# Performance work log

Hardware: AMD Instinct MI355X
Metric: run time of the kernel (lower is better)

## Reference

```python
import jax, jax.numpy as jnp
import numpy as np

N_NODES = 50000
N_EDGES = 3200000
N_GRAPHS = 50
IN_FEATS, HIDDEN, OUT_FEATS = 5, 64, 2


def setup_inputs() -> dict:
    key = jax.random.key(0)
    ks = jax.random.split(key, 10)
    x = jax.random.normal(ks[0], (N_NODES, IN_FEATS), dtype=jnp.float32)
    edge_index = jax.random.randint(ks[1], (2, N_EDGES), 0, N_NODES, dtype=jnp.int64)
    edge_attr = jax.random.uniform(ks[2], (N_EDGES, 1), dtype=jnp.float32)
    batch = jnp.sort(jax.random.randint(ks[3], (N_NODES,), 0, N_GRAPHS, dtype=jnp.int64))
    s1 = 1.0 / np.sqrt(IN_FEATS)
    s2 = 1.0 / np.sqrt(HIDDEN)
    W1 = jax.random.uniform(ks[4], (IN_FEATS, HIDDEN), jnp.float32, -s1, s1)
    b1 = jnp.zeros((HIDDEN,), jnp.float32)
    W2 = jax.random.uniform(ks[5], (HIDDEN, HIDDEN), jnp.float32, -s2, s2)
    b2 = jnp.zeros((HIDDEN,), jnp.float32)
    Wo = jax.random.uniform(ks[6], (HIDDEN, OUT_FEATS), jnp.float32, -s2, s2)
    bo = jax.random.uniform(ks[7], (OUT_FEATS,), jnp.float32, -s2, s2)
    return {"x": x, "edge_index": edge_index, "edge_attr": edge_attr, "batch": batch,
            "W1": W1, "b1": b1, "W2": W2, "b2": b2, "Wo": Wo, "bo": bo}


def _gcn_conv(x, src, dst, ew, W, b):
    # symmetric normalization: D^{-1/2} (A + I) D^{-1/2}, weighted degrees
    deg = jax.ops.segment_sum(ew, dst, num_segments=N_NODES)
    dinv = jnp.where(deg > 0, jax.lax.rsqrt(jnp.where(deg > 0, deg, 1.0)), 0.0)
    norm = dinv[src] * ew * dinv[dst]  # [E+N]
    h = x @ W                           # transform before propagate (PyG order)
    msg = h[src] * norm[:, None]        # gather + scale per edge
    out = jax.ops.segment_sum(msg, dst, num_segments=N_NODES)
    return out + b


def reference(x, edge_index, edge_attr, batch, W1, b1, W2, b2, Wo, bo):
    ew = edge_attr.squeeze(-1)
    loop = jnp.arange(N_NODES, dtype=edge_index.dtype)  # add self-loops (GCNConv default)
    src = jnp.concatenate([edge_index[0], loop])
    dst = jnp.concatenate([edge_index[1], loop])
    ew = jnp.concatenate([ew, jnp.ones((N_NODES,), ew.dtype)])
    h = jax.nn.relu(_gcn_conv(x, src, dst, ew, W1, b1))
    h = jax.nn.relu(_gcn_conv(h, src, dst, ew, W2, b2))
    # global mean pool over graphs
    sums = jax.ops.segment_sum(h, batch, num_segments=N_GRAPHS)
    cnt = jax.ops.segment_sum(jnp.ones((N_NODES,), h.dtype), batch, num_segments=N_GRAPHS)
    pooled = sums / jnp.maximum(cnt, 1.0)[:, None]
    return pooled @ Wo + bo  # [N_GRAPHS, OUT_FEATS]
```

## Files before the change

kernel.cpp:

```cpp
#include <hip/hip_runtime.h>
#include <hip/hip_fp16.h>

#define N_NODES 50000
#define N_EDGES 3200000
#define N_GRAPHS 50
#define IN_F 5
#define HID 64
#define OUT_F 2

#define BK2_SHIFT 7
#define BK2_W 128
#define NBKT2 391
#define NB1 250
#define EPB 12800
#define CAP2 9216
#define NBIN2 128
#define NWAVE 8192

__global__ void k_bhist(const int* dst, unsigned short* cw) {
    __shared__ int hist[NBKT2];
    int t = threadIdx.x, blk = blockIdx.x;
    for (int b = t; b < NBKT2; b += 1024) hist[b] = 0;
    __syncthreads();
    int base = blk * EPB;
    for (int k = t; k < EPB; k += 1024)
        atomicAdd(&hist[dst[base + k] >> BK2_SHIFT], 1);
    __syncthreads();
    for (int b = t; b < NBKT2; b += 1024)
        cw[b * NB1 + blk] = (unsigned short)hist[b];
}

__global__ void k_bscanA(unsigned short* cw, int* total) {
    __shared__ int s[256];
    int t = threadIdx.x, b = blockIdx.x;
    int v = (t < NB1) ? (int)cw[b * NB1 + t] : 0;
    s[t] = v;
    __syncthreads();
    for (int off = 1; off < 256; off <<= 1) {
        int a = (t >= off) ? s[t - off] : 0;
        __syncthreads();
        s[t] += a;
        __syncthreads();
    }
    if (t < NB1) cw[b * NB1 + t] = (unsigned short)(s[t] - v);
    if (t == 255) total[b] = s[255];
}

__global__ void k_bscanB(const int* total, int* rpB) {
    __shared__ int s[256];
    int t = threadIdx.x;
    int v[2], sum = 0;
#pragma unroll
    for (int j = 0; j < 2; ++j) {
        int idx = t * 2 + j;
        v[j] = (idx < NBKT2) ? total[idx] : 0;
        sum += v[j];
    }
    s[t] = sum;
    __syncthreads();
    for (int off = 1; off < 256; off <<= 1) {
        int a = (t >= off) ? s[t - off] : 0;
        __syncthreads();
        s[t] += a;
        __syncthreads();
    }
    int run = s[t] - sum;
#pragma unroll
    for (int j = 0; j < 2; ++j) {
        int idx = t * 2 + j;
        if (idx < NBKT2) rpB[idx] = run;
        run += v[j];
    }
    if (t == 0) rpB[NBKT2] = N_EDGES;
}

__global__ void k_bucket(const int* src, const int* dst, const float* ew,
                         const unsigned short* cw, const int* rpB,
                         int* key4, unsigned short* wh2) {
    __shared__ int base[NBKT2];
    __shared__ int off[NBKT2];
    int t = threadIdx.x, blk = blockIdx.x;
    for (int b = t; b < NBKT2; b += 1024) {
        base[b] = (int)cw[b * NB1 + blk] + rpB[b];
        off[b] = 0;
    }
    __syncthreads();
    int ebase = blk * EPB;
    for (int k = t; k < EPB; k += 1024) {
        int idx = ebase + k;
        int d = dst[idx];
        int b = d >> BK2_SHIFT;
        int sl = base[b] + atomicAdd(&off[b], 1);
        key4[sl] = src[idx] | ((d & (BK2_W - 1)) << 16);
        wh2[sl] = __half_as_ushort(__float2half(ew[idx]));
    }
}

__global__ __launch_bounds__(1024) void k_bsort2(const int* rpB, int* key4,
                      const unsigned short* wh2, const float* x,
                      int* rp2, int* rp2e, float* dinv, __half* xp) {
    __shared__ int keybuf[CAP2];
    __shared__ unsigned short whbuf[CAP2];
    __shared__ int hist[NBIN2];
    __shared__ int binoff[NBIN2];
    __shared__ int s[NBIN2];
    __shared__ float wd[NBIN2];
    int t = threadIdx.x, b = blockIdx.x;
    int e0 = rpB[b], cnt = rpB[b + 1] - e0;
    if (t < NBIN2) { hist[t] = 0; wd[t] = 0.f; }
    __syncthreads();
    for (int k = t; k < cnt; k += 1024) {
        int u = key4[e0 + k];
        unsigned short wh = wh2[e0 + k];
        keybuf[k] = u; whbuf[k] = wh;
        int dl = (u >> 16) & (BK2_W - 1);
        atomicAdd(&hist[dl], 1);
        atomicAdd(&wd[dl], __half2float(__ushort_as_half(wh)));
    }
    __syncthreads();
    if (t < NBIN2) s[t] = hist[t];
    __syncthreads();
    for (int off = 1; off < NBIN2; off <<= 1) {
        int a = (t < NBIN2 && t >= off) ? s[t - off] : 0;
        __syncthreads();
        if (t < NBIN2) s[t] += a;
        __syncthreads();
    }
    if (t < NBIN2) {
        binoff[t] = s[t] - hist[t];
        int node = (b << BK2_SHIFT) + t;
        if (node < N_NODES) {
            rp2[node]  = e0 + s[t] - hist[t];
            rp2e[node] = e0 + s[t];
            float di = rsqrtf(1.0f + wd[t]);
            dinv[node] = di;
            const float* xi = &x[node * IN_F];
            __half* o = &xp[node * 8];
#pragma unroll
            for (int f = 0; f < IN_F; ++f) o[f] = __float2half(xi[f] * di);
            o[5] = o[6] = o[7] = __float2half(0.f);
        }
    }
    __syncthreads();
    for (int k = t; k < cnt; k += 1024) {
        int u = keybuf[k];
        int dl = (u >> 16) & (BK2_W - 1);
        int pos = atomicAdd(&binoff[dl], 1);
        key4[e0 + pos] = (u & 0xFFFF) | ((int)whbuf[k] << 16);
    }
}

__global__ void k_p(const int* rp2, const int* rp2e, const int* pk,
                    const __half* xp, const float* dinv, float* p) {
    int node = blockIdx.x * 4 + (threadIdx.x >> 6);
    int lane = threadIdx.x & 63;
    if (node >= N_NODES) return;
    int b = rp2[node], en = rp2e[node];
    float a0 = 0.f, a1 = 0.f, a2 = 0.f, a3 = 0.f, a4 = 0.f;
    for (int k = b + lane; k < en; k += 64) {
        int e = pk[k];
        float w = __half2float(__ushort_as_half((unsigned short)((unsigned)e >> 16)));
        const __half* xs = &xp[(e & 0xFFFF) * 8];
        int4 xv = *reinterpret_cast<const int4*>(xs);
        __half2 p01 = *(__half2*)&xv.x;
        __half2 p23 = *(__half2*)&xv.y;
        __half2 p45 = *(__half2*)&xv.z;
        a0 += w * __half2float(p01.x); a1 += w * __half2float(p01.y);
        a2 += w * __half2float(p23.x); a3 += w * __half2float(p23.y);
        a4 += w * __half2float(p45.x);
    }
    for (int off = 32; off; off >>= 1) {
        a0 += __shfl_down(a0, off); a1 += __shfl_down(a1, off); a2 += __shfl_down(a2, off);
        a3 += __shfl_down(a3, off); a4 += __shfl_down(a4, off);
    }
    if (lane == 0) {
        float di = dinv[node];
        const __half* xn = &xp[node * 8];
        float* pp = &p[node * IN_F];
        pp[0] = di * (a0 + __half2float(xn[0]));
        pp[1] = di * (a1 + __half2float(xn[1]));
        pp[2] = di * (a2 + __half2float(xn[2]));
        pp[3] = di * (a3 + __half2float(xn[3]));
        pp[4] = di * (a4 + __half2float(xn[4]));
    }
}

__global__ void k_h1g(const float* p, const float* W1, const float* b1,
                      const float* W2, const float* dinv,
                      unsigned char* g8u, float* rs) {
    __shared__ float W1s[IN_F * HID];
    __shared__ float W2s[HID * HID];
    __shared__ float b1s[HID];
    int t = threadIdx.x;
    for (int k = t; k < IN_F * HID; k += 256) W1s[k] = W1[k];
    for (int k = t; k < HID * HID; k += 256) W2s[k] = W2[k];
    if (t < HID) b1s[t] = b1[t];
    __syncthreads();
    int lane = t & 63;
    int wid = blockIdx.x * 4 + (t >> 6);
    int nw = gridDim.x * 4;
    for (int node = wid; node < N_NODES; node += nw) {
        const float* pp = &p[node * IN_F];
        float pv0 = pp[0], pv1 = pp[1], pv2 = pp[2], pv3 = pp[3], pv4 = pp[4];
        float h = b1s[lane] + pv0 * W1s[lane] + pv1 * W1s[64 + lane] + pv2 * W1s[128 + lane]
                + pv3 * W1s[192 + lane] + pv4 * W1s[256 + lane];
        h = fmaxf(h, 0.f);
        float acc = 0.f;
#pragma unroll
        for (int f = 0; f < HID; ++f) {
            float hf = __int_as_float(__builtin_amdgcn_readlane(__float_as_int(h), f));
            acc += hf * W2s[f * HID + lane];
        }
        float gv = acc * dinv[node];
        float am = fabsf(gv);
        for (int off = 32; off; off >>= 1) am = fmaxf(am, __shfl_xor(am, off));
        float inv = (am > 0.f) ? 127.0f / am : 0.f;
        g8u[node * HID + lane] = (unsigned char)(__float2int_rn(gv * inv) + 128);
        if (lane == 0) rs[node] = (am > 0.f) ? am * (1.0f / 127.0f) : 0.f;
    }
}

#define EDGE4_BODY(UU)                                                         \
    {                                                                          \
        int u_ = (UU);                                                         \
        float w_ = __half2float(__ushort_as_half((unsigned short)((unsigned)u_ >> 16))); \
        float wwv_ = w_ * rs[u_ & 0xFFFF];                                     \
        unsigned dw_ = *(const unsigned*)&g8u[(u_ & 0xFFFF) * HID + fo];       \
        a0 += wwv_ * (float)(dw_ & 0xFF);                                      \
        a1 += wwv_ * (float)((dw_ >> 8) & 0xFF);                               \
        a2 += wwv_ * (float)((dw_ >> 16) & 0xFF);                              \
        a3 += wwv_ * (float)(dw_ >> 24);                                       \
        sww += wwv_;                                                           \
    }

__global__ __launch_bounds__(256, 8) void k_h2g(const int* rp2, const int* rp2e,
                      const int* pk, const float* dinv, const unsigned char* g8u,
                      const float* rs, const float* b2, const int* batch, float* pool) {
    int t = threadIdx.x, lane = t & 63;
    int grp = lane >> 4;
    int fo = (lane & 15) << 2;
    int wid = blockIdx.x * 4 + (t >> 6);
    int n0 = (int)(((long long)wid * N_NODES) / NWAVE);
    int n1 = (int)(((long long)(wid + 1) * N_NODES) / NWAVE);
    if (n0 >= n1) return;
    float4 bj = *reinterpret_cast<const float4*>(&b2[fo]);
    float p0 = 0.f, p1 = 0.f, p2 = 0.f, p3 = 0.f;
    int cur = batch[n0];
    for (int node = n0; node < n1; ++node) {
        unsigned dws = *(const unsigned*)&g8u[node * HID + fo];
        float wq4 = 0.25f * rs[node];
        float a0 = wq4 * (float)(dws & 0xFF);
        float a1 = wq4 * (float)((dws >> 8) & 0xFF);
        float a2 = wq4 * (float)((dws >> 16) & 0xFF);
        float a3 = wq4 * (float)(dws >> 24);
        float sww = wq4;
        for (int k0 = rp2[node], e1 = rp2e[node]; k0 < e1; k0 += 64) {
            int kk = k0 + lane;
            int ev = (kk < e1) ? pk[kk] : 0;
            int m = e1 - k0; if (m > 64) m = 64;
            if (m == 64) {
#pragma unroll
                for (int q = 0; q < 16; ++q) EDGE4_BODY(__shfl(ev, (q << 2) | grp))
            } else {
                int ng = (m + 3) >> 2;
                for (int q = 0; q < ng; ++q) EDGE4_BODY(__shfl(ev, (q << 2) | grp))
            }
        }
#pragma unroll
        for (int off = 16; off <= 32; off <<= 1) {
            a0 += __shfl_xor(a0, off); a1 += __shfl_xor(a1, off);
            a2 += __shfl_xor(a2, off); a3 += __shfl_xor(a3, off);
            sww += __shfl_xor(sww, off);
        }
        float di = dinv[node];
        float corr = 128.0f * sww;
        float h0 = fmaxf(di * (a0 - corr) + bj.x, 0.f);
        float h1 = fmaxf(di * (a1 - corr) + bj.y, 0.f);
        float h2 = fmaxf(di * (a2 - corr) + bj.z, 0.f);
        float h3 = fmaxf(di * (a3 - corr) + bj.w, 0.f);
        int bb = batch[node];
        if (bb != cur) {
            if (lane < 16) {
                float* pb = &pool[cur * HID + fo];
                atomicAdd(pb + 0, p0); atomicAdd(pb + 1, p1);
                atomicAdd(pb + 2, p2); atomicAdd(pb + 3, p3);
            }
            cur = bb;
            p0 = p1 = p2 = p3 = 0.f;
        }
        p0 += h0; p1 += h1; p2 += h2; p3 += h3;
    }
    if (lane < 16) {
        float* pb = &pool[cur * HID + fo];
        atomicAdd(pb + 0, p0); atomicAdd(pb + 1, p1);
        atomicAdd(pb + 2, p2); atomicAdd(pb + 3, p3);
    }
}

__device__ int lowb(const int* a, int n, int v) {
    int lo = 0, hi = n;
    while (lo < hi) { int m = (lo + hi) >> 1; if (a[m] < v) lo = m + 1; else hi = m; }
    return lo;
}

__global__ void k_out(const float* pool, const int* batch, const float* Wo,
                      const float* bo, float* out) {
    int t = blockIdx.x * blockDim.x + threadIdx.x;
    if (t < N_GRAPHS * OUT_F) {
        int gi = t / OUT_F, k = t % OUT_F;
        int c = lowb(batch, N_NODES, gi + 1) - lowb(batch, N_NODES, gi);
        float cf = fmaxf((float)c, 1.0f);
        float acc = bo[k];
        for (int f = 0; f < HID; ++f)
            acc += (pool[gi * HID + f] / cf) * Wo[f * OUT_F + k];
        out[t] = acc;
    }
}

extern "C" void kernel_launch(void* const* d_in, const int* in_sizes, int n_in,
                              void* d_out, int out_size, void* d_ws, size_t ws_size,
                              hipStream_t stream) {
    const float* x   = (const float*)d_in[0];
    const int*   ei  = (const int*)d_in[1];
    const float* ea  = (const float*)d_in[2];
    const int*   bat = (const int*)d_in[3];
    const float* W1  = (const float*)d_in[4];
    const float* b1  = (const float*)d_in[5];
    const float* W2  = (const float*)d_in[6];
    const float* b2  = (const float*)d_in[7];
    const float* Wo  = (const float*)d_in[8];
    const float* bo  = (const float*)d_in[9];
    float* out = (float*)d_out;

    const int* src = ei;
    const int* dst = ei + N_EDGES;

    float* ws = (float*)d_ws;
    int*   rpB   = (int*)ws;
    int*   rp2   = (int*)(ws + 400);
    int*   rp2e  = (int*)(ws + 50416);
    float* dinv  = ws + 100432;
    float* rs    = ws + 150448;
    float* pool  = ws + 200464;
    int*   total = (int*)(ws + 200464);
    float* p     = ws + 203664;
    unsigned short* cw = (unsigned short*)(ws + 203664);
    int*   key4  = (int*)(ws + 453664);
    unsigned short* wh2 = (unsigned short*)(ws + 3653664);
    unsigned char* g8u = (unsigned char*)(ws + 5253664);
    __half* xp   = (__half*)(ws + 6053664);

    k_bhist <<<NB1, 1024, 0, stream>>>(dst, cw);
    k_bscanA<<<NBKT2, 256, 0, stream>>>(cw, total);
    k_bscanB<<<1, 256, 0, stream>>>(total, rpB);
    hipMemsetAsync(pool, 0, N_GRAPHS * HID * sizeof(float), stream);
    k_bucket<<<NB1, 1024, 0, stream>>>(src, dst, ea, cw, rpB, key4, wh2);
    k_bsort2<<<NBKT2, 1024, 0, stream>>>(rpB, key4, wh2, x, rp2, rp2e, dinv, xp);
    k_p     <<<(N_NODES + 3) / 4, 256, 0, stream>>>(rp2, rp2e, key4, xp, dinv, p);
    k_h1g   <<<1024, 256, 0, stream>>>(p, W1, b1, W2, dinv, g8u, rs);
    k_h2g   <<<NWAVE / 4, 256, 0, stream>>>(rp2, rp2e, key4, dinv, g8u, rs, b2, bat, pool);
    k_out   <<<1, 128, 0, stream>>>(pool, bat, Wo, bo, out);
}
```

Before: 305.2 us.

## Replace per-block bucket offset scan with atomic cursors and tiled local sort

The per-block histogram matrix and its column scan kernel are removed. Global bucket totals are now accumulated with atomics, and each bucketing block reserves its output ranges through atomic cursors. Each 6400-edge tile is locally sorted in shared memory before writing, so global stores for each bucket land in contiguous runs. This drops one kernel launch and the cw traffic and makes the scatter more coalesced. In exchange it adds atomic contention on the cursors, and edge order within a bucket becomes nondeterministic. The key packing now stores the full dst in the high bits and uses an unsigned shift.

```diff
diff --git a/kernel.cpp b/kernel.cpp
--- a/kernel.cpp
+++ b/kernel.cpp
@@ -13,40 +13,28 @@
 #define NBKT2 391
 #define NB1 250
 #define EPB 12800
+#define TILE 6400
+#define SLOTS 7
 #define CAP2 9216
 #define NBIN2 128
 #define NWAVE 8192
 
-__global__ void k_bhist(const int* dst, unsigned short* cw) {
+__global__ __launch_bounds__(1024) void k_bhist(const int* dst, int* total) {
     __shared__ int hist[NBKT2];
     int t = threadIdx.x, blk = blockIdx.x;
     for (int b = t; b < NBKT2; b += 1024) hist[b] = 0;
     __syncthreads();
     int base = blk * EPB;
     for (int k = t; k < EPB; k += 1024)
-        atomicAdd(&hist[dst[base + k] >> BK2_SHIFT], 1);
-    __syncthreads();
-    for (int b = t; b < NBKT2; b += 1024)
-        cw[b * NB1 + blk] = (unsigned short)hist[b];
-}
-
-__global__ void k_bscanA(unsigned short* cw, int* total) {
-    __shared__ int s[256];
-    int t = threadIdx.x, b = blockIdx.x;
-    int v = (t < NB1) ? (int)cw[b * NB1 + t] : 0;
-    s[t] = v;
-    __syncthreads();
-    for (int off = 1; off < 256; off <<= 1) {
-        int a = (t >= off) ? s[t - off] : 0;
-        __syncthreads();
-        s[t] += a;
-        __syncthreads();
-    }
-    if (t < NB1) cw[b * NB1 + t] = (unsigned short)(s[t] - v);
-    if (t == 255) total[b] = s[255];
-}
-
-__global__ void k_bscanB(const int* total, int* rpB) {
+        atomicAdd(&hist[__builtin_nontemporal_load(&dst[base + k]) >> BK2_SHIFT], 1);
+    __syncthreads();
+    for (int b = t; b < NBKT2; b += 1024) {
+        int h = hist[b];
+        if (h) atomicAdd(&total[b], h);
+    }
+}
+
+__global__ void k_bscanB(const int* total, int* rpB, int* cursor) {
     __shared__ int s[256];
     int t = threadIdx.x;
     int v[2], sum = 0;
@@ -68,31 +56,76 @@
 #pragma unroll
     for (int j = 0; j < 2; ++j) {
         int idx = t * 2 + j;
-        if (idx < NBKT2) rpB[idx] = run;
+        if (idx < NBKT2) { rpB[idx] = run; cursor[idx] = run; }
         run += v[j];
     }
     if (t == 0) rpB[NBKT2] = N_EDGES;
 }
 
-__global__ void k_bucket(const int* src, const int* dst, const float* ew,
-                         const unsigned short* cw, const int* rpB,
-                         int* key4, unsigned short* wh2) {
-    __shared__ int base[NBKT2];
-    __shared__ int off[NBKT2];
+__global__ __launch_bounds__(1024) void k_bucket(const int* src, const int* dst,
+                        const float* ew, int* cursor, int* key4, unsigned short* wh2) {
+    __shared__ int keyb[TILE];
+    __shared__ unsigned short whb[TILE];
+    __shared__ int hist[NBKT2];
+    __shared__ int soff[NBKT2];
+    __shared__ int delta[NBKT2];
+    __shared__ int s[512];
     int t = threadIdx.x, blk = blockIdx.x;
-    for (int b = t; b < NBKT2; b += 1024) {
-        base[b] = (int)cw[b * NB1 + blk] + rpB[b];
-        off[b] = 0;
-    }
-    __syncthreads();
-    int ebase = blk * EPB;
-    for (int k = t; k < EPB; k += 1024) {
-        int idx = ebase + k;
-        int d = dst[idx];
-        int b = d >> BK2_SHIFT;
-        int sl = base[b] + atomicAdd(&off[b], 1);
-        key4[sl] = src[idx] | ((d & (BK2_W - 1)) << 16);
-        wh2[sl] = __half_as_ushort(__float2half(ew[idx]));
+    for (int tile = 0; tile < EPB / TILE; ++tile) {
+        int base = blk * EPB + tile * TILE;
+        for (int b = t; b < NBKT2; b += 1024) hist[b] = 0;
+        __syncthreads();
+        int ky[SLOTS]; unsigned short wv[SLOTS]; int rk[SLOTS];
+#pragma unroll
+        for (int i = 0; i < SLOTS; ++i) {
+            int k = t + i * 1024;
+            if (k < TILE) {
+                int d  = __builtin_nontemporal_load(&dst[base + k]);
+                int sv = __builtin_nontemporal_load(&src[base + k]);
+                float w = __builtin_nontemporal_load(&ew[base + k]);
+                ky[i] = sv | (d << 16);
+                wv[i] = __half_as_ushort(__float2half(w));
+                rk[i] = atomicAdd(&hist[d >> BK2_SHIFT], 1);
+            }
+        }
+        __syncthreads();
+        if (t < 512) s[t] = (t < NBKT2) ? hist[t] : 0;
+        __syncthreads();
+        for (int off = 1; off < 512; off <<= 1) {
+            int a = (t < 512 && t >= off) ? s[t - off] : 0;
+            __syncthreads();
+            if (t < 512) s[t] += a;
+            __syncthreads();
+        }
+        if (t < NBKT2) {
+            int h = hist[t];
+            soff[t] = s[t] - h;
+            if (h) delta[t] = atomicAdd(&cursor[t], h) - soff[t];
+        }
+        __syncthreads();
+#pragma unroll
+        for (int i = 0; i < SLOTS; ++i) {
+            int k = t + i * 1024;
+            if (k < TILE) {
+                int b = ((unsigned)ky[i] >> 16) >> BK2_SHIFT;
+                int p = soff[b] + rk[i];
+                keyb[p] = ky[i];
+                whb[p] = wv[i];
+            }
+        }
+        __syncthreads();
+#pragma unroll
+        for (int i = 0; i < SLOTS; ++i) {
+            int k = t + i * 1024;
+            if (k < TILE) {
+                int u = keyb[k];
+                int b = ((unsigned)u >> 16) >> BK2_SHIFT;
+                int gp = k + delta[b];
+                key4[gp] = u;
+                wh2[gp] = whb[k];
+            }
+        }
+        __syncthreads();
     }
 }
 
@@ -113,7 +146,7 @@
         int u = key4[e0 + k];
         unsigned short wh = wh2[e0 + k];
         keybuf[k] = u; whbuf[k] = wh;
-        int dl = (u >> 16) & (BK2_W - 1);
+        int dl = ((unsigned)u >> 16) & (BK2_W - 1);
         atomicAdd(&hist[dl], 1);
         atomicAdd(&wd[dl], __half2float(__ushort_as_half(wh)));
     }
@@ -144,7 +177,7 @@
     __syncthreads();
     for (int k = t; k < cnt; k += 1024) {
         int u = keybuf[k];
-        int dl = (u >> 16) & (BK2_W - 1);
+        int dl = ((unsigned)u >> 16) & (BK2_W - 1);
         int pos = atomicAdd(&binoff[dl], 1);
         key4[e0 + pos] = (u & 0xFFFF) | ((int)whbuf[k] << 16);
     }
@@ -336,25 +369,26 @@
     const int* dst = ei + N_EDGES;
 
     float* ws = (float*)d_ws;
-    int*   rpB   = (int*)ws;
-    int*   rp2   = (int*)(ws + 400);
-    int*   rp2e  = (int*)(ws + 50416);
-    float* dinv  = ws + 100432;
-    float* rs    = ws + 150448;
-    float* pool  = ws + 200464;
-    int*   total = (int*)(ws + 200464);
-    float* p     = ws + 203664;
-    unsigned short* cw = (unsigned short*)(ws + 203664);
-    int*   key4  = (int*)(ws + 453664);
-    unsigned short* wh2 = (unsigned short*)(ws + 3653664);
-    unsigned char* g8u = (unsigned char*)(ws + 5253664);
-    __half* xp   = (__half*)(ws + 6053664);
-
-    k_bhist <<<NB1, 1024, 0, stream>>>(dst, cw);
-    k_bscanA<<<NBKT2, 256, 0, stream>>>(cw, total);
-    k_bscanB<<<1, 256, 0, stream>>>(total, rpB);
+    int*   rpB    = (int*)ws;
+    int*   cursor = (int*)(ws + 400);
+    int*   rp2    = (int*)(ws + 800);
+    int*   rp2e   = (int*)(ws + 50816);
+    float* dinv   = ws + 100832;
+    float* rs     = ws + 150848;
+    float* pool   = ws + 200864;
+    int*   total  = (int*)(ws + 204064);
+    float* p      = ws + 204464;
+    int*   key4   = (int*)(ws + 454464);
+    unsigned short* wh2 = (unsigned short*)(ws + 3654464);
+    unsigned char* g8u = (unsigned char*)(ws + 5254464);
+    __half* xp    = (__half*)(ws + 6054464);
+
+    hipMemsetAsync(total, 0, NBKT2 * sizeof(int), stream);
     hipMemsetAsync(pool, 0, N_GRAPHS * HID * sizeof(float), stream);
-    k_bucket<<<NB1, 1024, 0, stream>>>(src, dst, ea, cw, rpB, key4, wh2);
+
+    k_bhist <<<NB1, 1024, 0, stream>>>(dst, total);
+    k_bscanB<<<1, 256, 0, stream>>>(total, rpB, cursor);
+    k_bucket<<<NB1, 1024, 0, stream>>>(src, dst, ea, cursor, key4, wh2);
     k_bsort2<<<NBKT2, 1024, 0, stream>>>(rpB, key4, wh2, x, rp2, rp2e, dinv, xp);
     k_p     <<<(N_NODES + 3) / 4, 256, 0, stream>>>(rp2, rp2e, key4, xp, dinv, p);
     k_h1g   <<<1024, 256, 0, stream>>>(p, W1, b1, W2, dinv, g8u, rs);
```

Measured after the change: 288.2 us. -5.5%, faster.
